# Optimization experiments

Measured on AMD Instinct MI355X. Metric: run time of the kernel, lower is better.

The kernel has to match this reference:

```python
import jax, jax.numpy as jnp
import numpy as np

B, S, N1, N2 = 4096, 1024, 4096, 16384

def setup_inputs() -> dict:
    key = jax.random.key(0)
    k1, k2, k3, k4, k5, k6, k7 = jax.random.split(key, 7)
    return {
        "y_in": jax.random.uniform(k1, (B, S), dtype=jnp.float32),
        "rate_1": jax.random.uniform(k2, (B, N1), dtype=jnp.float32),
        "rate_2": jax.random.uniform(k3, (B, N2), dtype=jnp.float32),
        "inds_1r": jax.random.randint(k4, (N1,), 0, S, dtype=jnp.int32),
        "inds_1p": jax.random.randint(k5, (N1,), 0, S, dtype=jnp.int32),
        "inds_2r": jax.random.randint(k6, (N2, 2), 0, S, dtype=jnp.int32),
        "inds_2p": jax.random.randint(k7, (N2,), 0, S, dtype=jnp.int32),
    }

def reference(y_in, rate_1, rate_2, inds_1r, inds_1p, inds_2r, inds_2p):
    # First-order reactions: gather one reactant, multiply by rate, scatter to product.
    term_1 = y_in[:, inds_1r] * rate_1                      # [B, N1]
    # Second-order: product of two reactant abundances times rate.
    term_2 = y_in[:, inds_2r[:, 0]] * y_in[:, inds_2r[:, 1]] * rate_2  # [B, N2]
    y_out = jnp.zeros_like(y_in)
    y_out = y_out.at[:, inds_1p].add(term_1)
    y_out = y_out.at[:, inds_2p].add(term_2)
    return y_out
```

## Files before the change

### kernel.cpp

```cpp
#include <hip/hip_runtime.h>


typedef __attribute__((ext_vector_type(8))) _Float16 half8;

#define SWL(k) ((k) ^ (((k) >> 3) & 7))

__global__ __launch_bounds__(1024) void setup_kernel(
    const int* __restrict__ i1p, const int* __restrict__ i2p,
    unsigned short* __restrict__ pos1, unsigned short* __restrict__ pos2,
    unsigned* __restrict__ segpack) {
    __shared__ int h[1024];
    __shared__ int c[1024];
    const int tid = threadIdx.x;
    const int ch  = blockIdx.x;
    const int* __restrict__ ip = (ch < 2) ? (i1p + ch * 2048)
                                          : (i2p + (ch - 2) * 2048);
    unsigned short* __restrict__ pos = (ch < 2) ? (pos1 + ch * 2048)
                                                : (pos2 + (ch - 2) * 2048);

    h[tid] = 0;
    __syncthreads();
    const int t0 = ip[2 * tid], t1 = ip[2 * tid + 1];
    atomicAdd(&h[t0], 1);
    atomicAdd(&h[t1], 1);
    __syncthreads();
    int n = h[tid];
    c[tid] = n;
    __syncthreads();
    for (int d = 1; d < 1024; d <<= 1) {
        int t = (tid >= d) ? c[tid - d] : 0;
        __syncthreads();
        if (tid >= d) c[tid] += t;
        __syncthreads();
    }
    int start = c[tid] - n;
    segpack[ch * 1024 + tid] = (unsigned)start | ((unsigned)n << 16);
    __syncthreads();
    c[tid] = start;
    __syncthreads();
    int p0 = atomicAdd(&c[t0], 1);
    int p1 = atomicAdd(&c[t1], 1);
    pos[2 * tid]     = (unsigned short)SWL(p0);
    pos[2 * tid + 1] = (unsigned short)SWL(p1);
}

__global__ __launch_bounds__(1024, 8) void reaction_gather8(
    const float* __restrict__ y_in, const float* __restrict__ rate_1,
    const float* __restrict__ rate_2,
    const int* __restrict__ i1r, const int* __restrict__ i2r,
    const unsigned short* __restrict__ pos1, const unsigned short* __restrict__ pos2,
    const unsigned* __restrict__ segpack,
    float* __restrict__ y_out) {
    __shared__ half8 y_s[1024];
    __shared__ half8 buf[2][2048];

    const int tid = threadIdx.x;
    const long b0 = (long)blockIdx.x * 8;
    const float* __restrict__ r1b = rate_1 + b0 * 4096;
    const float* __restrict__ r2b = rate_2 + b0 * 16384;

    float acc[8] = {0.f, 0.f, 0.f, 0.f, 0.f, 0.f, 0.f, 0.f};

#define LOAD_PH1(C)                                                            \
    int2     ia = ((const int2*)(i1r + (C) * 2048))[tid];                      \
    unsigned pp = ((const unsigned*)(pos1 + (C) * 2048))[tid];                 \
    float2 q[8];                                                               \
    _Pragma("unroll")                                                          \
    for (int r = 0; r < 8; ++r)                                                \
        q[r] = ((const float2*)(r1b + r * 4096 + (C) * 2048))[tid];

#define WRITE_PH1(P)                                                           \
    {                                                                          \
        half8 va = y_s[ia.x], vb = y_s[ia.y];                                  \
        half8 p0, p1;                                                          \
        _Pragma("unroll")                                                      \
        for (int r = 0; r < 8; ++r) {                                          \
            p0[r] = (_Float16)((float)va[r] * q[r].x);                         \
            p1[r] = (_Float16)((float)vb[r] * q[r].y);                         \
        }                                                                      \
        buf[P][pp & 0xffffu] = p0;                                             \
        buf[P][pp >> 16]     = p1;                                             \
    }

#define LOAD_PH2(C)                                                            \
    int4     e  = ((const int4*)(i2r + (C) * 4096))[tid];                      \
    unsigned pp = ((const unsigned*)(pos2 + (C) * 2048))[tid];                 \
    float2 q[8];                                                               \
    _Pragma("unroll")                                                          \
    for (int r = 0; r < 8; ++r)                                                \
        q[r] = ((const float2*)(r2b + r * 16384 + (C) * 2048))[tid];

#define WRITE_PH2(P)                                                           \
    {                                                                          \
        half8 a0 = y_s[e.x], c0 = y_s[e.y];                                    \
        half8 a1 = y_s[e.z], c1 = y_s[e.w];                                    \
        half8 p0, p1;                                                          \
        _Pragma("unroll")                                                      \
        for (int r = 0; r < 8; ++r) {                                          \
            p0[r] = (_Float16)((float)a0[r] * (float)c0[r] * q[r].x);          \
            p1[r] = (_Float16)((float)a1[r] * (float)c1[r] * q[r].y);          \
        }                                                                      \
        buf[P][pp & 0xffffu] = p0;                                             \
        buf[P][pp >> 16]     = p1;                                             \
    }

#define SUM(CH, P)                                                             \
    {                                                                          \
        unsigned sp = segpack[(CH) * 1024 + tid];                              \
        int s = (int)(sp & 0xffffu), n = (int)(sp >> 16);                      \
        for (int k = s; k < s + n; ++k) {                                      \
            half8 v = buf[P][SWL(k)];                                          \
            _Pragma("unroll")                                                  \
            for (int r = 0; r < 8; ++r) acc[r] += (float)v[r];                 \
        }                                                                      \
    }

#define B_ __syncthreads()

    {
        LOAD_PH1(0)
        half8 hy;
#pragma unroll
        for (int r = 0; r < 8; ++r)
            hy[r] = (_Float16)y_in[(b0 + r) * 1024 + tid];
        y_s[tid] = hy;
        B_;
        WRITE_PH1(0)
    }
    B_;
    { LOAD_PH1(1) SUM(0, 0) WRITE_PH1(1) }  B_;
    { LOAD_PH2(0) SUM(1, 1) WRITE_PH2(0) }  B_;
    { LOAD_PH2(1) SUM(2, 0) WRITE_PH2(1) }  B_;
    { LOAD_PH2(2) SUM(3, 1) WRITE_PH2(0) }  B_;
    { LOAD_PH2(3) SUM(4, 0) WRITE_PH2(1) }  B_;
    { LOAD_PH2(4) SUM(5, 1) WRITE_PH2(0) }  B_;
    { LOAD_PH2(5) SUM(6, 0) WRITE_PH2(1) }  B_;
    { LOAD_PH2(6) SUM(7, 1) WRITE_PH2(0) }  B_;
    { LOAD_PH2(7) SUM(8, 0) WRITE_PH2(1) }  B_;
    SUM(9, 1)

#pragma unroll
    for (int r = 0; r < 8; ++r)
        y_out[(b0 + r) * 1024 + tid] = acc[r];

#undef LOAD_PH1
#undef WRITE_PH1
#undef LOAD_PH2
#undef WRITE_PH2
#undef SUM
#undef B_
}

template <int BLOCK>
__global__ __launch_bounds__(BLOCK) void reaction_fallback(
    const float* __restrict__ y_in, const float* __restrict__ rate_1,
    const float* __restrict__ rate_2, const int* __restrict__ inds_1r,
    const int* __restrict__ inds_1p, const int* __restrict__ inds_2r,
    const int* __restrict__ inds_2p, float* __restrict__ y_out,
    int S, int N1, int N2) {
    extern __shared__ float smem[];
    float* y_s = smem;
    float* acc = smem + S;
    const int b = blockIdx.x, tid = threadIdx.x;
    const float* yrow = y_in + (size_t)b * S;
    for (int i = tid; i < S; i += BLOCK) { y_s[i] = yrow[i]; acc[i] = 0.f; }
    __syncthreads();
    const float* r1 = rate_1 + (size_t)b * N1;
    for (int i = tid; i < N1; i += BLOCK)
        atomicAdd(&acc[inds_1p[i]], y_s[inds_1r[i]] * r1[i]);
    const float* r2 = rate_2 + (size_t)b * N2;
    for (int i = tid; i < N2; i += BLOCK)
        atomicAdd(&acc[inds_2p[i]], y_s[inds_2r[2 * i]] * y_s[inds_2r[2 * i + 1]] * r2[i]);
    __syncthreads();
    float* orow = y_out + (size_t)b * S;
    for (int i = tid; i < S; i += BLOCK) orow[i] = acc[i];
}

extern "C" void kernel_launch(void* const* d_in, const int* in_sizes, int n_in,
                              void* d_out, int out_size, void* d_ws, size_t ws_size,
                              hipStream_t stream) {
    const float* y_in    = (const float*)d_in[0];
    const float* rate_1  = (const float*)d_in[1];
    const float* rate_2  = (const float*)d_in[2];
    const int*   inds_1r = (const int*)d_in[3];
    const int*   inds_1p = (const int*)d_in[4];
    const int*   inds_2r = (const int*)d_in[5];
    const int*   inds_2p = (const int*)d_in[6];
    float*       y_out   = (float*)d_out;

    const int N1 = in_sizes[3];
    const int N2 = in_sizes[6];
    const int B  = in_sizes[1] / N1;
    const int S  = in_sizes[0] / B;

    const bool specialized = (S == 1024 && N1 == 4096 && N2 == 16384 &&
                              (B % 8) == 0 && ws_size >= (size_t)(80 * 1024));
    if (!specialized) {
        size_t smem = (size_t)2 * S * sizeof(float);
        reaction_fallback<256><<<B, 256, smem, stream>>>(
            y_in, rate_1, rate_2, inds_1r, inds_1p, inds_2r, inds_2p,
            y_out, S, N1, N2);
        return;
    }

    char* ws = (char*)d_ws;
    unsigned*       segpack = (unsigned*)(ws + 0);
    unsigned short* pos1    = (unsigned short*)(ws + 40 * 1024);
    unsigned short* pos2    = (unsigned short*)(ws + 48 * 1024);

    setup_kernel<<<10, 1024, 0, stream>>>(inds_1p, inds_2p, pos1, pos2, segpack);
    reaction_gather8<<<B / 8, 1024, 0, stream>>>(y_in, rate_1, rate_2,
                                                 inds_1r, inds_2r, pos1, pos2,
                                                 segpack, y_out);
}
```

Before: 83.98 us.

## Process 4 batch rows per block with 4096-reaction chunks and wave-shuffle scan

The main kernel now handles 4 batch rows per block using half4 vectors and chunks of 4096 reactions, which cuts the pipeline from 10 stages to 5 and widens the global loads to float4. The setup kernel builds 5 chunks of 4096 entries and replaces its shared-memory Hillis-Steele scan with wave shuffles plus a small cross-wave scan. The intent is fewer barriers, wider coalesced loads and twice as many blocks for better occupancy. The trade-off is that each y_s row is reused across 4 rows instead of 8, so there are twice as many index and segpack loads per output row, and the LDS footprint changes.

```diff
diff --git a/kernel.cpp b/kernel.cpp
--- a/kernel.cpp
+++ b/kernel.cpp
@@ -1,7 +1,7 @@
 #include <hip/hip_runtime.h>
 
 
-typedef __attribute__((ext_vector_type(8))) _Float16 half8;
+typedef __attribute__((ext_vector_type(4))) _Float16 half4;
 
 #define SWL(k) ((k) ^ (((k) >> 3) & 7))
 
@@ -10,98 +10,140 @@
     unsigned short* __restrict__ pos1, unsigned short* __restrict__ pos2,
     unsigned* __restrict__ segpack) {
     __shared__ int h[1024];
-    __shared__ int c[1024];
+    __shared__ int wsum[16];
     const int tid = threadIdx.x;
     const int ch  = blockIdx.x;
-    const int* __restrict__ ip = (ch < 2) ? (i1p + ch * 2048)
-                                          : (i2p + (ch - 2) * 2048);
-    unsigned short* __restrict__ pos = (ch < 2) ? (pos1 + ch * 2048)
-                                                : (pos2 + (ch - 2) * 2048);
+    const int* __restrict__ ip = (ch == 0) ? i1p : (i2p + (ch - 1) * 4096);
+    unsigned short* __restrict__ pos = (ch == 0) ? pos1 : (pos2 + (ch - 1) * 4096);
 
     h[tid] = 0;
     __syncthreads();
-    const int t0 = ip[2 * tid], t1 = ip[2 * tid + 1];
-    atomicAdd(&h[t0], 1);
-    atomicAdd(&h[t1], 1);
-    __syncthreads();
-    int n = h[tid];
-    c[tid] = n;
-    __syncthreads();
-    for (int d = 1; d < 1024; d <<= 1) {
-        int t = (tid >= d) ? c[tid - d] : 0;
-        __syncthreads();
-        if (tid >= d) c[tid] += t;
-        __syncthreads();
-    }
-    int start = c[tid] - n;
+    const int4 t4 = ((const int4*)ip)[tid];
+    atomicAdd(&h[t4.x], 1);
+    atomicAdd(&h[t4.y], 1);
+    atomicAdd(&h[t4.z], 1);
+    atomicAdd(&h[t4.w], 1);
+    __syncthreads();
+    const int n = h[tid];
+
+    const int lane = tid & 63, w = tid >> 6;
+    int v = n;
+#pragma unroll
+    for (int d = 1; d < 64; d <<= 1) {
+        int t = __shfl_up(v, d, 64);
+        if (lane >= d) v += t;
+    }
+    if (lane == 63) wsum[w] = v;
+    __syncthreads();
+    if (tid < 16) {
+        int s = wsum[tid];
+#pragma unroll
+        for (int d = 1; d < 16; d <<= 1) {
+            int t = __shfl_up(s, d, 64);
+            if (tid >= d) s += t;
+        }
+        wsum[tid] = s;
+    }
+    __syncthreads();
+    const int start = ((w ? wsum[w - 1] : 0) + v) - n;
     segpack[ch * 1024 + tid] = (unsigned)start | ((unsigned)n << 16);
     __syncthreads();
-    c[tid] = start;
-    __syncthreads();
-    int p0 = atomicAdd(&c[t0], 1);
-    int p1 = atomicAdd(&c[t1], 1);
-    pos[2 * tid]     = (unsigned short)SWL(p0);
-    pos[2 * tid + 1] = (unsigned short)SWL(p1);
-}
-
-__global__ __launch_bounds__(1024, 8) void reaction_gather8(
+    h[tid] = start;
+    __syncthreads();
+    const int p0 = atomicAdd(&h[t4.x], 1);
+    const int p1 = atomicAdd(&h[t4.y], 1);
+    const int p2 = atomicAdd(&h[t4.z], 1);
+    const int p3 = atomicAdd(&h[t4.w], 1);
+    ushort4 o;
+    o.x = (unsigned short)SWL(p0);
+    o.y = (unsigned short)SWL(p1);
+    o.z = (unsigned short)SWL(p2);
+    o.w = (unsigned short)SWL(p3);
+    ((ushort4*)pos)[tid] = o;
+}
+
+__global__ __launch_bounds__(1024, 8) void reaction_gather4h(
     const float* __restrict__ y_in, const float* __restrict__ rate_1,
     const float* __restrict__ rate_2,
     const int* __restrict__ i1r, const int* __restrict__ i2r,
     const unsigned short* __restrict__ pos1, const unsigned short* __restrict__ pos2,
     const unsigned* __restrict__ segpack,
     float* __restrict__ y_out) {
-    __shared__ half8 y_s[1024];
-    __shared__ half8 buf[2][2048];
+    __shared__ half4 y_s[1024];
+    __shared__ half4 buf[2][4096];
 
     const int tid = threadIdx.x;
-    const long b0 = (long)blockIdx.x * 8;
+    const long b0 = (long)blockIdx.x * 4;
     const float* __restrict__ r1b = rate_1 + b0 * 4096;
     const float* __restrict__ r2b = rate_2 + b0 * 16384;
 
-    float acc[8] = {0.f, 0.f, 0.f, 0.f, 0.f, 0.f, 0.f, 0.f};
-
-#define LOAD_PH1(C)                                                            \
-    int2     ia = ((const int2*)(i1r + (C) * 2048))[tid];                      \
-    unsigned pp = ((const unsigned*)(pos1 + (C) * 2048))[tid];                 \
-    float2 q[8];                                                               \
-    _Pragma("unroll")                                                          \
-    for (int r = 0; r < 8; ++r)                                                \
-        q[r] = ((const float2*)(r1b + r * 4096 + (C) * 2048))[tid];
+    float acc[4] = {0.f, 0.f, 0.f, 0.f};
+
+#define LOAD_PH1()                                                             \
+    int4    ia = ((const int4*)i1r)[tid];                                      \
+    ushort4 pp = ((const ushort4*)pos1)[tid];                                  \
+    float4 q0 = ((const float4*)(r1b         ))[tid];                          \
+    float4 q1 = ((const float4*)(r1b +  4096))[tid];                           \
+    float4 q2 = ((const float4*)(r1b +  8192))[tid];                           \
+    float4 q3 = ((const float4*)(r1b + 12288))[tid];
 
 #define WRITE_PH1(P)                                                           \
     {                                                                          \
-        half8 va = y_s[ia.x], vb = y_s[ia.y];                                  \
-        half8 p0, p1;                                                          \
-        _Pragma("unroll")                                                      \
-        for (int r = 0; r < 8; ++r) {                                          \
-            p0[r] = (_Float16)((float)va[r] * q[r].x);                         \
-            p1[r] = (_Float16)((float)vb[r] * q[r].y);                         \
-        }                                                                      \
-        buf[P][pp & 0xffffu] = p0;                                             \
-        buf[P][pp >> 16]     = p1;                                             \
+        half4 yv, pr;                                                          \
+        yv = y_s[ia.x];                                                        \
+        pr[0] = (_Float16)((float)yv[0] * q0.x); pr[1] = (_Float16)((float)yv[1] * q1.x); \
+        pr[2] = (_Float16)((float)yv[2] * q2.x); pr[3] = (_Float16)((float)yv[3] * q3.x); \
+        buf[P][pp.x] = pr;                                                     \
+        yv = y_s[ia.y];                                                        \
+        pr[0] = (_Float16)((float)yv[0] * q0.y); pr[1] = (_Float16)((float)yv[1] * q1.y); \
+        pr[2] = (_Float16)((float)yv[2] * q2.y); pr[3] = (_Float16)((float)yv[3] * q3.y); \
+        buf[P][pp.y] = pr;                                                     \
+        yv = y_s[ia.z];                                                        \
+        pr[0] = (_Float16)((float)yv[0] * q0.z); pr[1] = (_Float16)((float)yv[1] * q1.z); \
+        pr[2] = (_Float16)((float)yv[2] * q2.z); pr[3] = (_Float16)((float)yv[3] * q3.z); \
+        buf[P][pp.z] = pr;                                                     \
+        yv = y_s[ia.w];                                                        \
+        pr[0] = (_Float16)((float)yv[0] * q0.w); pr[1] = (_Float16)((float)yv[1] * q1.w); \
+        pr[2] = (_Float16)((float)yv[2] * q2.w); pr[3] = (_Float16)((float)yv[3] * q3.w); \
+        buf[P][pp.w] = pr;                                                     \
     }
 
 #define LOAD_PH2(C)                                                            \
-    int4     e  = ((const int4*)(i2r + (C) * 4096))[tid];                      \
-    unsigned pp = ((const unsigned*)(pos2 + (C) * 2048))[tid];                 \
-    float2 q[8];                                                               \
-    _Pragma("unroll")                                                          \
-    for (int r = 0; r < 8; ++r)                                                \
-        q[r] = ((const float2*)(r2b + r * 16384 + (C) * 2048))[tid];
+    int4    e0 = ((const int4*)(i2r + (C) * 8192))[2 * tid];        \
+    int4    e1 = ((const int4*)(i2r + (C) * 8192))[2 * tid + 1];    \
+    ushort4 pp = ((const ushort4*)(pos2 + (C) * 4096))[tid];                   \
+    float4 q0 = ((const float4*)(r2b + (C) * 4096         ))[tid];             \
+    float4 q1 = ((const float4*)(r2b + (C) * 4096 + 16384))[tid];              \
+    float4 q2 = ((const float4*)(r2b + (C) * 4096 + 32768))[tid];              \
+    float4 q3 = ((const float4*)(r2b + (C) * 4096 + 49152))[tid];
 
 #define WRITE_PH2(P)                                                           \
     {                                                                          \
-        half8 a0 = y_s[e.x], c0 = y_s[e.y];                                    \
-        half8 a1 = y_s[e.z], c1 = y_s[e.w];                                    \
-        half8 p0, p1;                                                          \
-        _Pragma("unroll")                                                      \
-        for (int r = 0; r < 8; ++r) {                                          \
-            p0[r] = (_Float16)((float)a0[r] * (float)c0[r] * q[r].x);          \
-            p1[r] = (_Float16)((float)a1[r] * (float)c1[r] * q[r].y);          \
-        }                                                                      \
-        buf[P][pp & 0xffffu] = p0;                                             \
-        buf[P][pp >> 16]     = p1;                                             \
+        half4 ya, yb, pr;                                                      \
+        ya = y_s[e0.x]; yb = y_s[e0.y];                                        \
+        pr[0] = (_Float16)((float)ya[0] * (float)yb[0] * q0.x);                \
+        pr[1] = (_Float16)((float)ya[1] * (float)yb[1] * q1.x);                \
+        pr[2] = (_Float16)((float)ya[2] * (float)yb[2] * q2.x);                \
+        pr[3] = (_Float16)((float)ya[3] * (float)yb[3] * q3.x);                \
+        buf[P][pp.x] = pr;                                                     \
+        ya = y_s[e0.z]; yb = y_s[e0.w];                                        \
+        pr[0] = (_Float16)((float)ya[0] * (float)yb[0] * q0.y);                \
+        pr[1] = (_Float16)((float)ya[1] * (float)yb[1] * q1.y);                \
+        pr[2] = (_Float16)((float)ya[2] * (float)yb[2] * q2.y);                \
+        pr[3] = (_Float16)((float)ya[3] * (float)yb[3] * q3.y);                \
+        buf[P][pp.y] = pr;                                                     \
+        ya = y_s[e1.x]; yb = y_s[e1.y];                                        \
+        pr[0] = (_Float16)((float)ya[0] * (float)yb[0] * q0.z);                \
+        pr[1] = (_Float16)((float)ya[1] * (float)yb[1] * q1.z);                \
+        pr[2] = (_Float16)((float)ya[2] * (float)yb[2] * q2.z);                \
+        pr[3] = (_Float16)((float)ya[3] * (float)yb[3] * q3.z);                \
+        buf[P][pp.z] = pr;                                                     \
+        ya = y_s[e1.z]; yb = y_s[e1.w];                                        \
+        pr[0] = (_Float16)((float)ya[0] * (float)yb[0] * q0.w);                \
+        pr[1] = (_Float16)((float)ya[1] * (float)yb[1] * q1.w);                \
+        pr[2] = (_Float16)((float)ya[2] * (float)yb[2] * q2.w);                \
+        pr[3] = (_Float16)((float)ya[3] * (float)yb[3] * q3.w);                \
+        buf[P][pp.w] = pr;                                                     \
     }
 
 #define SUM(CH, P)                                                             \
@@ -109,38 +151,33 @@
         unsigned sp = segpack[(CH) * 1024 + tid];                              \
         int s = (int)(sp & 0xffffu), n = (int)(sp >> 16);                      \
         for (int k = s; k < s + n; ++k) {                                      \
-            half8 v = buf[P][SWL(k)];                                          \
-            _Pragma("unroll")                                                  \
-            for (int r = 0; r < 8; ++r) acc[r] += (float)v[r];                 \
+            half4 v = buf[P][SWL(k)];                                          \
+            acc[0] += (float)v[0]; acc[1] += (float)v[1];                      \
+            acc[2] += (float)v[2]; acc[3] += (float)v[3];                      \
         }                                                                      \
     }
 
 #define B_ __syncthreads()
 
     {
-        LOAD_PH1(0)
-        half8 hy;
-#pragma unroll
-        for (int r = 0; r < 8; ++r)
+        LOAD_PH1()
+        half4 hy;
+#pragma unroll
+        for (int r = 0; r < 4; ++r)
             hy[r] = (_Float16)y_in[(b0 + r) * 1024 + tid];
         y_s[tid] = hy;
         B_;
         WRITE_PH1(0)
     }
     B_;
-    { LOAD_PH1(1) SUM(0, 0) WRITE_PH1(1) }  B_;
-    { LOAD_PH2(0) SUM(1, 1) WRITE_PH2(0) }  B_;
-    { LOAD_PH2(1) SUM(2, 0) WRITE_PH2(1) }  B_;
-    { LOAD_PH2(2) SUM(3, 1) WRITE_PH2(0) }  B_;
-    { LOAD_PH2(3) SUM(4, 0) WRITE_PH2(1) }  B_;
-    { LOAD_PH2(4) SUM(5, 1) WRITE_PH2(0) }  B_;
-    { LOAD_PH2(5) SUM(6, 0) WRITE_PH2(1) }  B_;
-    { LOAD_PH2(6) SUM(7, 1) WRITE_PH2(0) }  B_;
-    { LOAD_PH2(7) SUM(8, 0) WRITE_PH2(1) }  B_;
-    SUM(9, 1)
-
-#pragma unroll
-    for (int r = 0; r < 8; ++r)
+    { LOAD_PH2(0) SUM(0, 0) WRITE_PH2(1) }  B_;
+    { LOAD_PH2(1) SUM(1, 1) WRITE_PH2(0) }  B_;
+    { LOAD_PH2(2) SUM(2, 0) WRITE_PH2(1) }  B_;
+    { LOAD_PH2(3) SUM(3, 1) WRITE_PH2(0) }  B_;
+    SUM(4, 0)
+
+#pragma unroll
+    for (int r = 0; r < 4; ++r)
         y_out[(b0 + r) * 1024 + tid] = acc[r];
 
 #undef LOAD_PH1
@@ -194,7 +231,7 @@
     const int S  = in_sizes[0] / B;
 
     const bool specialized = (S == 1024 && N1 == 4096 && N2 == 16384 &&
-                              (B % 8) == 0 && ws_size >= (size_t)(80 * 1024));
+                              (B % 4) == 0 && ws_size >= (size_t)(60 * 1024));
     if (!specialized) {
         size_t smem = (size_t)2 * S * sizeof(float);
         reaction_fallback<256><<<B, 256, smem, stream>>>(
@@ -205,11 +242,11 @@
 
     char* ws = (char*)d_ws;
     unsigned*       segpack = (unsigned*)(ws + 0);
-    unsigned short* pos1    = (unsigned short*)(ws + 40 * 1024);
-    unsigned short* pos2    = (unsigned short*)(ws + 48 * 1024);
-
-    setup_kernel<<<10, 1024, 0, stream>>>(inds_1p, inds_2p, pos1, pos2, segpack);
-    reaction_gather8<<<B / 8, 1024, 0, stream>>>(y_in, rate_1, rate_2,
-                                                 inds_1r, inds_2r, pos1, pos2,
-                                                 segpack, y_out);
-}
+    unsigned short* pos1    = (unsigned short*)(ws + 20 * 1024);
+    unsigned short* pos2    = (unsigned short*)(ws + 28 * 1024);
+
+    setup_kernel<<<5, 1024, 0, stream>>>(inds_1p, inds_2p, pos1, pos2, segpack);
+    reaction_gather4h<<<B / 4, 1024, 0, stream>>>(y_in, rate_1, rate_2,
+                                                  inds_1r, inds_2r, pos1, pos2,
+                                                  segpack, y_out);
+}
```

After: 79.42 us. -5.4%, faster.
